# Performance work log

Hardware: AMD Instinct MI355X
Metric: run time of the kernel (lower is better)

Reference implementation:

```python
import jax, jax.numpy as jnp
import numpy as np

NUM_EMBEDDINGS = 8192
EMBEDDING_DIM = 256


def setup_inputs() -> dict:
    key = jax.random.key(0)
    k1, k2 = jax.random.split(key)
    z = jax.random.normal(k1, (16, EMBEDDING_DIM, 32, 32), dtype=jnp.float32)
    # nn.Embedding default init: N(0, 1)
    emb_table = jax.random.normal(k2, (NUM_EMBEDDINGS, EMBEDDING_DIM), dtype=jnp.float32)
    return {"z": z, "emb_table": emb_table}


def reference(z, emb_table):
    # z: [B, D, H, W]; emb_table: [K, D]
    B, D, H, W = z.shape
    # flatten to per-token vectors: [B*H*W, D]
    zf = z.reshape(B, D, H * W).transpose(0, 2, 1).reshape(B * H * W, D)
    Wt = jax.lax.stop_gradient(emb_table)  # original detaches W for distance
    # argmin of mean squared distance == argmin of squared distance;
    # expand ||z - w||^2 = ||z||^2 - 2 z.w + ||w||^2 (avoid (N,K,D) expansion)
    z_sq = jnp.sum(zf * zf, axis=-1, keepdims=True)          # [N, 1]
    w_sq = jnp.sum(Wt * Wt, axis=-1)                          # [K]
    dists = z_sq - 2.0 * (zf @ Wt.T) + w_sq                   # [N, K]
    token_ids = jnp.argmin(dists, axis=-1)                    # [N]
    quantized = emb_table[token_ids]                          # [N, D] (differentiable gather)
    return quantized.reshape(B, H * W, D).transpose(0, 2, 1).reshape(B, D, H, W)
```

## Files before the change

### kernel.cpp

```cpp
#include <hip/hip_runtime.h>
#include <stdint.h>

#define DIM 256
#define NEMB 8192
#define NTOK 16384
#define HW 1024

typedef __attribute__((ext_vector_type(4))) int int4v;

__device__ __forceinline__ void async_cp16(void* lds, const void* g) {
  __builtin_amdgcn_global_load_lds(
      (const __attribute__((address_space(1))) unsigned int*)g,
      (__attribute__((address_space(3))) unsigned int*)lds, 16, 0, 0);
}
__device__ __forceinline__ int q0_of(float x) {
  int q = __float2int_rn(x * 20.0f);
  return q > 127 ? 127 : (q < -127 ? -127 : q);
}
__device__ __forceinline__ int q1_of(float x, int q0) {
  float e = x * 20.0f - (float)q0;
  int q = __float2int_rn(e * 128.0f);
  return q > 127 ? 127 : (q < -127 ? -127 : q);
}
__device__ __forceinline__ unsigned int pack4(int a, int b, int c, int d) {
  return (unsigned int)(a & 0xff) | ((unsigned int)(b & 0xff) << 8) |
         ((unsigned int)(c & 0xff) << 16) | ((unsigned int)(d & 0xff) << 24);
}
__device__ __forceinline__ unsigned int med3u(unsigned int a, unsigned int b,
                                              unsigned int c) {
  unsigned int m;
  asm("v_med3_u32 %0, %1, %2, %3" : "=v"(m) : "v"(a), "v"(b), "v"(c));
  return m;
}
__device__ __forceinline__ void top3_insert(unsigned int v, unsigned int& m1,
                                            unsigned int& m2, unsigned int& m3) {
  unsigned int t2 = med3u(v, m1, m2);
  unsigned int t3 = med3u(v, m2, m3);
  m1 = v < m1 ? v : m1;
  m2 = t2;
  m3 = t3;
}

__global__ __launch_bounds__(256) void prep_kernel(
    const float* __restrict__ emb, unsigned int* __restrict__ q0w,
    unsigned int* __restrict__ q1w, int* __restrict__ iwsq2,
    const float* __restrict__ z, unsigned int* __restrict__ q0z) {
  __shared__ float tile[64][65];
  int tid = threadIdx.x;
  int lane = tid & 63;
  if (blockIdx.x < 2048) {
    int row = blockIdx.x * 4 + (tid >> 6);
    const float4 v = *(const float4*)(emb + (size_t)row * DIM + lane * 4);
    float s = v.x * v.x + v.y * v.y + v.z * v.z + v.w * v.w;
    int a0 = q0_of(v.x), b0 = q0_of(v.y), c0 = q0_of(v.z), d0 = q0_of(v.w);
    q0w[row * (DIM / 4) + lane] = pack4(a0, b0, c0, d0);
    q1w[row * (DIM / 4) + lane] =
        pack4(q1_of(v.x, a0), q1_of(v.y, b0), q1_of(v.z, c0), q1_of(v.w, d0));
#pragma unroll
    for (int off = 32; off > 0; off >>= 1) s += __shfl_xor(s, off, 64);
    if (lane == 0) iwsq2[row] = (int)rintf(s * 25600.0f) + 8192;
    return;
  }
  int idx = blockIdx.x - 2048;
  int b = idx >> 6, d0 = ((idx >> 4) & 3) * 64, hw0 = (idx & 15) * 64;
  int grp = tid >> 6;
  const float* src = z + (size_t)b * DIM * HW + hw0 + lane;
#pragma unroll
  for (int i = 0; i < 16; i++) {
    int dl = grp + i * 4;
    tile[dl][lane] = src[(size_t)(d0 + dl) * HW];
  }
  __syncthreads();
  int dq = tid & 15;
#pragma unroll
  for (int p = 0; p < 4; p++) {
    int n = (tid >> 4) + p * 16;
    int a0 = q0_of(tile[dq * 4 + 0][n]), b0 = q0_of(tile[dq * 4 + 1][n]);
    int c0 = q0_of(tile[dq * 4 + 2][n]), e0 = q0_of(tile[dq * 4 + 3][n]);
    int token = b * HW + hw0 + n;
    q0z[(size_t)token * (DIM / 4) + (d0 >> 2) + dq] = pack4(a0, b0, c0, e0);
  }
}

__global__ __launch_bounds__(256, 3) void gemm_topk_kernel(
    const signed char* __restrict__ q0z, const signed char* __restrict__ q0w,
    const signed char* __restrict__ q1w, const int* __restrict__ iwsq2,
    uint4* __restrict__ partials) {
  __shared__ __align__(16) signed char sB[2][4][32 * 128];

  const int bid = blockIdx.x;
  const int kq = bid & 7;
  const int tg = bid >> 3;
  const int tid = threadIdx.x;
  const int lane = tid & 63, w = tid >> 6;
  const int c = lane & 15, quad = lane >> 4;
  const int n0 = tg * 128;
  const int k0g = kq * 1024;

  int4v af0[2][4];
#pragma unroll
  for (int t = 0; t < 2; t++) {
    const size_t arow = (size_t)(n0 + w * 32 + t * 16 + c) * DIM;
#pragma unroll
    for (int s = 0; s < 4; s++)
      af0[t][s] = *(const int4v*)(q0z + arow + s * 64 + quad * 16);
  }

  const int srow = tid >> 3;
  const int scl = ((tid & 7) ^ (srow & 7)) * 16;
  const signed char* p0 = q0w + (size_t)(k0g + srow) * DIM + scl;
  const signed char* p1 = q1w + (size_t)(k0g + srow) * DIM + scl;
  async_cp16(&sB[0][0][tid * 16], p0);
  async_cp16(&sB[0][1][tid * 16], p0 + 128);
  async_cp16(&sB[0][2][tid * 16], p1);
  async_cp16(&sB[0][3][tid * 16], p1 + 128);
  p0 += 32 * DIM;
  p1 += 32 * DIM;
  __syncthreads();

  unsigned int m1[8], m2[8], m3[8];
#pragma unroll
  for (int i = 0; i < 8; i++) {
    m1[i] = 0xFFFFFFFFu; m2[i] = 0xFFFFFFFFu; m3[i] = 0xFFFFFFFFu;
  }

  unsigned int idxA = (unsigned)(k0g + c);
  const int4v zero = {0, 0, 0, 0};

  for (int it = 0; it < 32; it++) {
    const int buf = it & 1;
    if (it + 1 < 32) {
      const int nb = buf ^ 1;
      async_cp16(&sB[nb][0][tid * 16], p0);
      async_cp16(&sB[nb][1][tid * 16], p0 + 128);
      async_cp16(&sB[nb][2][tid * 16], p1);
      async_cp16(&sB[nb][3][tid * 16], p1 + 128);
      p0 += 32 * DIM;
      p1 += 32 * DIM;
    }
    const int iw0 = iwsq2[k0g + it * 32 + c];
    const int iw1 = iwsq2[k0g + it * 32 + 16 + c];

    int4v b0a[4], b0b[4];
#pragma unroll
    for (int s = 0; s < 4; s++) {
      const int ph = ((((s & 1) << 2) + quad) ^ (c & 7)) * 16;
      b0a[s] = *(const int4v*)(&sB[buf][s >> 1][c * 128 + ph]);
      b0b[s] = *(const int4v*)(&sB[buf][s >> 1][(16 + c) * 128 + ph]);
    }
    int4v a[2][2];
#pragma unroll
    for (int t = 0; t < 2; t++) {
      a[t][0] = __builtin_amdgcn_mfma_i32_16x16x64_i8(af0[t][0], b0a[0], zero, 0, 0, 0);
      a[t][1] = __builtin_amdgcn_mfma_i32_16x16x64_i8(af0[t][0], b0b[0], zero, 0, 0, 0);
#pragma unroll
      for (int s = 1; s < 4; s++) {
        a[t][0] = __builtin_amdgcn_mfma_i32_16x16x64_i8(af0[t][s], b0a[s], a[t][0], 0, 0, 0);
        a[t][1] = __builtin_amdgcn_mfma_i32_16x16x64_i8(af0[t][s], b0b[s], a[t][1], 0, 0, 0);
      }
    }
#pragma unroll
    for (int t = 0; t < 2; t++)
#pragma unroll
      for (int cn = 0; cn < 2; cn++)
#pragma unroll
        for (int r = 0; r < 4; r++) a[t][cn][r] <<= 7;
#pragma unroll
    for (int s = 0; s < 4; s++) {
      const int ph = ((((s & 1) << 2) + quad) ^ (c & 7)) * 16;
      int4v b1a = *(const int4v*)(&sB[buf][2 + (s >> 1)][c * 128 + ph]);
      int4v b1b = *(const int4v*)(&sB[buf][2 + (s >> 1)][(16 + c) * 128 + ph]);
#pragma unroll
      for (int t = 0; t < 2; t++) {
        a[t][0] = __builtin_amdgcn_mfma_i32_16x16x64_i8(af0[t][s], b1a, a[t][0], 0, 0, 0);
        a[t][1] = __builtin_amdgcn_mfma_i32_16x16x64_i8(af0[t][s], b1b, a[t][1], 0, 0, 0);
      }
    }
#pragma unroll
    for (int t = 0; t < 2; t++) {
#pragma unroll
      for (int r = 0; r < 4; r++) {
        unsigned int s0 = (unsigned int)(iw0 - a[t][0][r]);
        unsigned int s1 = (unsigned int)(iw1 - a[t][1][r]);
        s0 = s0 < 0x2000000u ? s0 : 0x1FFFFFFu;
        s1 = s1 < 0x2000000u ? s1 : 0x1FFFFFFu;
        unsigned int pk0 = ((s0 << 7) & 0xFFFFE000u) | idxA;
        unsigned int pk1 = ((s1 << 7) & 0xFFFFE000u) | (idxA + 16);
        top3_insert(pk0 < pk1 ? pk0 : pk1, m1[t * 4 + r], m2[t * 4 + r],
                    m3[t * 4 + r]);
      }
    }
    idxA += 32;
    __syncthreads();
  }

#pragma unroll
  for (int ix = 0; ix < 8; ix++) {
    unsigned int a1 = m1[ix], a2 = m2[ix], a3 = m3[ix];
#pragma unroll
    for (int off = 1; off < 16; off <<= 1) {
      unsigned int o1 = __shfl_xor(a1, off, 16);
      unsigned int o2 = __shfl_xor(a2, off, 16);
      unsigned int o3 = __shfl_xor(a3, off, 16);
      top3_insert(o1, a1, a2, a3);
      top3_insert(o2, a1, a2, a3);
      top3_insert(o3, a1, a2, a3);
    }
    m1[ix] = a1; m2[ix] = a2; m3[ix] = a3;
  }
  if (c == 0) {
#pragma unroll
    for (int t = 0; t < 2; t++) {
#pragma unroll
      for (int r = 0; r < 4; r++) {
        int token = n0 + w * 32 + t * 16 + quad * 4 + r;
        partials[(size_t)kq * NTOK + token] =
            make_uint4(m1[t * 4 + r], m2[t * 4 + r], m3[t * 4 + r], 0xFFFFFFFFu);
      }
    }
  }
}

__global__ __launch_bounds__(256) void rescore_gather_kernel(
    const uint4* __restrict__ partials, const float* __restrict__ z,
    const float* __restrict__ emb, float* __restrict__ out) {
  __shared__ float tile[32][257];
  __shared__ int sid[32];
  __shared__ int wl[32];
  __shared__ int nwl;
  const int b = blockIdx.x >> 5;
  const int hw0 = (blockIdx.x & 31) * 32;
  const int tid = threadIdx.x;
  if (tid == 0) nwl = 0;
  __syncthreads();
  {
    const int tl = tid >> 3, sub = tid & 7;
    const int token = b * HW + hw0 + tl;
    uint4 e = partials[(size_t)sub * NTOK + token];
    unsigned int m = e.x < e.y ? e.x : e.y;
    m = e.z < m ? e.z : m;
#pragma unroll
    for (int off = 1; off < 8; off <<= 1) {
      unsigned int o = __shfl_xor(m, off, 8);
      m = o < m ? o : m;
    }
    const unsigned int thr = (m >> 13) + 1536;
    int cnt = (((e.x >> 13) <= thr) ? 1 : 0) + (((e.y >> 13) <= thr) ? 1 : 0) +
              (((e.z >> 13) <= thr) ? 1 : 0);
#pragma unroll
    for (int off = 1; off < 8; off <<= 1) cnt += __shfl_xor(cnt, off, 8);
    if (sub == 0) {
      if (cnt == 1) {
        sid[tl] = (int)(m & 0x1FFFu);
      } else {
        int i = atomicAdd(&nwl, 1);
        wl[i] = tl;
      }
    }
  }
  __syncthreads();
  {
    const int w = tid >> 6, lane = tid & 63;
    for (int i = w; i < nwl; i += 4) {
      const int tl = wl[i];
      const int token = b * HW + hw0 + tl;
      unsigned int p[24];
#pragma unroll
      for (int q = 0; q < 8; q++) {
        uint4 t = partials[(size_t)q * NTOK + token];
        p[q * 3] = t.x;
        p[q * 3 + 1] = t.y;
        p[q * 3 + 2] = t.z;
      }
      unsigned int smin = p[0];
#pragma unroll
      for (int q = 1; q < 24; q++) smin = p[q] < smin ? p[q] : smin;
      const unsigned int thr = (smin >> 13) + 1536;
      float zv[4];
#pragma unroll
      for (int j = 0; j < 4; j++)
        zv[j] = z[(size_t)b * DIM * HW + (size_t)(lane * 4 + j) * HW + hw0 + tl];
      double best = 1e300;
      int bid2 = NEMB;
#pragma unroll
      for (int q = 0; q < 24; q++) {
        if ((p[q] >> 13) <= thr) {
          int id = (int)(p[q] & 0x1FFFu);
          const float4 wv = *(const float4*)(emb + (size_t)id * DIM + lane * 4);
          double s = (double)wv.x * ((double)wv.x - 2.0 * (double)zv[0]) +
                     (double)wv.y * ((double)wv.y - 2.0 * (double)zv[1]) +
                     (double)wv.z * ((double)wv.z - 2.0 * (double)zv[2]) +
                     (double)wv.w * ((double)wv.w - 2.0 * (double)zv[3]);
#pragma unroll
          for (int off = 32; off > 0; off >>= 1) s += __shfl_xor(s, off, 64);
          if (s < best || (s == best && id < bid2)) {
            best = s;
            bid2 = id;
          }
        }
      }
      if (lane == 0) sid[tl] = bid2;
    }
  }
  __syncthreads();
  for (int i = 0; i < 32; i++)
    tile[i][tid] = emb[(size_t)sid[i] * DIM + tid];
  __syncthreads();
  int h = tid & 31, dg = tid >> 5;
  for (int i = 0; i < 32; i++) {
    int d = i * 8 + dg;
    out[(size_t)b * DIM * HW + (size_t)d * HW + hw0 + h] = tile[h][d];
  }
}

extern "C" void kernel_launch(void* const* d_in, const int* in_sizes, int n_in,
                              void* d_out, int out_size, void* d_ws, size_t ws_size,
                              hipStream_t stream) {
  const float* z = (const float*)d_in[0];
  const float* emb = (const float*)d_in[1];
  float* out = (float*)d_out;
  char* ws = (char*)d_ws;

  signed char* q0w = (signed char*)(ws);
  signed char* q1w = (signed char*)(ws + 2097152);
  signed char* q0z = (signed char*)(ws + 4194304);
  int* iwsq2 = (int*)(ws + 8388608);
  uint4* partials = (uint4*)(ws + 8421376);

  prep_kernel<<<dim3(3072), 256, 0, stream>>>(
      emb, (unsigned int*)q0w, (unsigned int*)q1w, iwsq2, z, (unsigned int*)q0z);
  gemm_topk_kernel<<<dim3(1024), 256, 0, stream>>>(q0z, q0w, q1w, iwsq2,
                                                   partials);
  rescore_gather_kernel<<<dim3(512), 256, 0, stream>>>(partials, z, emb, out);
}
```

Before: 167.8 us.

## Shrink per-wave GEMM tile to 16x16 and use 512-thread blocks

Reworks the int8 MFMA distance/top-3 kernel so each wave computes a single 16-token by 16-code tile instead of 2x2 tiles. Blocks grow to 512 threads (8 waves covering 128 tokens), and the codebook step per iteration shrinks to 16 codes with one async copy per thread, so there are twice as many iterations. The aim is lower register pressure and higher occupancy (launch bounds 512,8) to hide latency. The cost is less register reuse of the A and B fragments, more LDS reads per MFMA, and twice as many barriers.

```diff
diff --git a/kernel.cpp b/kernel.cpp
--- a/kernel.cpp
+++ b/kernel.cpp
@@ -82,11 +82,11 @@
   }
 }
 
-__global__ __launch_bounds__(256, 3) void gemm_topk_kernel(
+__global__ __launch_bounds__(512, 8) void gemm_topk_kernel(
     const signed char* __restrict__ q0z, const signed char* __restrict__ q0w,
     const signed char* __restrict__ q1w, const int* __restrict__ iwsq2,
     uint4* __restrict__ partials) {
-  __shared__ __align__(16) signed char sB[2][4][32 * 128];
+  __shared__ __align__(16) signed char sB[2][4][16 * 128];
 
   const int bid = blockIdx.x;
   const int kq = bid & 7;
@@ -97,106 +97,75 @@
   const int n0 = tg * 128;
   const int k0g = kq * 1024;
 
-  int4v af0[2][4];
-#pragma unroll
-  for (int t = 0; t < 2; t++) {
-    const size_t arow = (size_t)(n0 + w * 32 + t * 16 + c) * DIM;
+  int4v af0[4];
+  {
+    const size_t arow = (size_t)(n0 + w * 16 + c) * DIM;
 #pragma unroll
     for (int s = 0; s < 4; s++)
-      af0[t][s] = *(const int4v*)(q0z + arow + s * 64 + quad * 16);
-  }
-
-  const int srow = tid >> 3;
-  const int scl = ((tid & 7) ^ (srow & 7)) * 16;
-  const signed char* p0 = q0w + (size_t)(k0g + srow) * DIM + scl;
-  const signed char* p1 = q1w + (size_t)(k0g + srow) * DIM + scl;
-  async_cp16(&sB[0][0][tid * 16], p0);
-  async_cp16(&sB[0][1][tid * 16], p0 + 128);
-  async_cp16(&sB[0][2][tid * 16], p1);
-  async_cp16(&sB[0][3][tid * 16], p1 + 128);
-  p0 += 32 * DIM;
-  p1 += 32 * DIM;
-  __syncthreads();
-
-  unsigned int m1[8], m2[8], m3[8];
-#pragma unroll
-  for (int i = 0; i < 8; i++) {
+      af0[s] = *(const int4v*)(q0z + arow + s * 64 + quad * 16);
+  }
+
+  const int arr = tid >> 7;
+  const int t2 = tid & 127;
+  const int srow = t2 >> 3;
+  const int scl = ((t2 & 7) ^ (srow & 7)) * 16;
+  const signed char* p = ((arr & 2) ? q1w : q0w) +
+                         (size_t)(k0g + srow) * DIM + (arr & 1) * 128 + scl;
+  async_cp16(&sB[0][arr][t2 * 16], p);
+  p += 16 * DIM;
+  __syncthreads();
+
+  unsigned int m1[4], m2[4], m3[4];
+#pragma unroll
+  for (int i = 0; i < 4; i++) {
     m1[i] = 0xFFFFFFFFu; m2[i] = 0xFFFFFFFFu; m3[i] = 0xFFFFFFFFu;
   }
 
   unsigned int idxA = (unsigned)(k0g + c);
   const int4v zero = {0, 0, 0, 0};
 
-  for (int it = 0; it < 32; it++) {
+  for (int it = 0; it < 64; it++) {
     const int buf = it & 1;
-    if (it + 1 < 32) {
-      const int nb = buf ^ 1;
-      async_cp16(&sB[nb][0][tid * 16], p0);
-      async_cp16(&sB[nb][1][tid * 16], p0 + 128);
-      async_cp16(&sB[nb][2][tid * 16], p1);
-      async_cp16(&sB[nb][3][tid * 16], p1 + 128);
-      p0 += 32 * DIM;
-      p1 += 32 * DIM;
-    }
-    const int iw0 = iwsq2[k0g + it * 32 + c];
-    const int iw1 = iwsq2[k0g + it * 32 + 16 + c];
-
-    int4v b0a[4], b0b[4];
+    if (it + 1 < 64) {
+      async_cp16(&sB[buf ^ 1][arr][t2 * 16], p);
+      p += 16 * DIM;
+    }
+    const int iw0 = iwsq2[k0g + it * 16 + c];
+
+    int4v acc;
+    {
+      const int ph0 = (quad ^ (c & 7)) * 16;
+      int4v b = *(const int4v*)(&sB[buf][0][c * 128 + ph0]);
+      acc = __builtin_amdgcn_mfma_i32_16x16x64_i8(af0[0], b, zero, 0, 0, 0);
+    }
+#pragma unroll
+    for (int s = 1; s < 4; s++) {
+      const int ph = ((((s & 1) << 2) + quad) ^ (c & 7)) * 16;
+      int4v b = *(const int4v*)(&sB[buf][s >> 1][c * 128 + ph]);
+      acc = __builtin_amdgcn_mfma_i32_16x16x64_i8(af0[s], b, acc, 0, 0, 0);
+    }
+#pragma unroll
+    for (int r = 0; r < 4; r++) acc[r] <<= 7;
 #pragma unroll
     for (int s = 0; s < 4; s++) {
       const int ph = ((((s & 1) << 2) + quad) ^ (c & 7)) * 16;
-      b0a[s] = *(const int4v*)(&sB[buf][s >> 1][c * 128 + ph]);
-      b0b[s] = *(const int4v*)(&sB[buf][s >> 1][(16 + c) * 128 + ph]);
-    }
-    int4v a[2][2];
-#pragma unroll
-    for (int t = 0; t < 2; t++) {
-      a[t][0] = __builtin_amdgcn_mfma_i32_16x16x64_i8(af0[t][0], b0a[0], zero, 0, 0, 0);
-      a[t][1] = __builtin_amdgcn_mfma_i32_16x16x64_i8(af0[t][0], b0b[0], zero, 0, 0, 0);
-#pragma unroll
-      for (int s = 1; s < 4; s++) {
-        a[t][0] = __builtin_amdgcn_mfma_i32_16x16x64_i8(af0[t][s], b0a[s], a[t][0], 0, 0, 0);
-        a[t][1] = __builtin_amdgcn_mfma_i32_16x16x64_i8(af0[t][s], b0b[s], a[t][1], 0, 0, 0);
-      }
-    }
-#pragma unroll
-    for (int t = 0; t < 2; t++)
-#pragma unroll
-      for (int cn = 0; cn < 2; cn++)
-#pragma unroll
-        for (int r = 0; r < 4; r++) a[t][cn][r] <<= 7;
-#pragma unroll
-    for (int s = 0; s < 4; s++) {
-      const int ph = ((((s & 1) << 2) + quad) ^ (c & 7)) * 16;
-      int4v b1a = *(const int4v*)(&sB[buf][2 + (s >> 1)][c * 128 + ph]);
-      int4v b1b = *(const int4v*)(&sB[buf][2 + (s >> 1)][(16 + c) * 128 + ph]);
-#pragma unroll
-      for (int t = 0; t < 2; t++) {
-        a[t][0] = __builtin_amdgcn_mfma_i32_16x16x64_i8(af0[t][s], b1a, a[t][0], 0, 0, 0);
-        a[t][1] = __builtin_amdgcn_mfma_i32_16x16x64_i8(af0[t][s], b1b, a[t][1], 0, 0, 0);
-      }
-    }
-#pragma unroll
-    for (int t = 0; t < 2; t++) {
-#pragma unroll
-      for (int r = 0; r < 4; r++) {
-        unsigned int s0 = (unsigned int)(iw0 - a[t][0][r]);
-        unsigned int s1 = (unsigned int)(iw1 - a[t][1][r]);
-        s0 = s0 < 0x2000000u ? s0 : 0x1FFFFFFu;
-        s1 = s1 < 0x2000000u ? s1 : 0x1FFFFFFu;
-        unsigned int pk0 = ((s0 << 7) & 0xFFFFE000u) | idxA;
-        unsigned int pk1 = ((s1 << 7) & 0xFFFFE000u) | (idxA + 16);
-        top3_insert(pk0 < pk1 ? pk0 : pk1, m1[t * 4 + r], m2[t * 4 + r],
-                    m3[t * 4 + r]);
-      }
-    }
-    idxA += 32;
+      int4v b = *(const int4v*)(&sB[buf][2 + (s >> 1)][c * 128 + ph]);
+      acc = __builtin_amdgcn_mfma_i32_16x16x64_i8(af0[s], b, acc, 0, 0, 0);
+    }
+#pragma unroll
+    for (int r = 0; r < 4; r++) {
+      unsigned int s0 = (unsigned int)(iw0 - acc[r]);
+      s0 = s0 < 0x2000000u ? s0 : 0x1FFFFFFu;
+      unsigned int pk = ((s0 << 7) & 0xFFFFE000u) | idxA;
+      top3_insert(pk, m1[r], m2[r], m3[r]);
+    }
+    idxA += 16;
     __syncthreads();
   }
 
 #pragma unroll
-  for (int ix = 0; ix < 8; ix++) {
-    unsigned int a1 = m1[ix], a2 = m2[ix], a3 = m3[ix];
+  for (int r = 0; r < 4; r++) {
+    unsigned int a1 = m1[r], a2 = m2[r], a3 = m3[r];
 #pragma unroll
     for (int off = 1; off < 16; off <<= 1) {
       unsigned int o1 = __shfl_xor(a1, off, 16);
@@ -206,17 +175,14 @@
       top3_insert(o2, a1, a2, a3);
       top3_insert(o3, a1, a2, a3);
     }
-    m1[ix] = a1; m2[ix] = a2; m3[ix] = a3;
+    m1[r] = a1; m2[r] = a2; m3[r] = a3;
   }
   if (c == 0) {
 #pragma unroll
-    for (int t = 0; t < 2; t++) {
-#pragma unroll
-      for (int r = 0; r < 4; r++) {
-        int token = n0 + w * 32 + t * 16 + quad * 4 + r;
-        partials[(size_t)kq * NTOK + token] =
-            make_uint4(m1[t * 4 + r], m2[t * 4 + r], m3[t * 4 + r], 0xFFFFFFFFu);
-      }
+    for (int r = 0; r < 4; r++) {
+      int token = n0 + w * 16 + quad * 4 + r;
+      partials[(size_t)kq * NTOK + token] =
+          make_uint4(m1[r], m2[r], m3[r], 0xFFFFFFFFu);
     }
   }
 }
@@ -329,7 +295,7 @@
 
   prep_kernel<<<dim3(3072), 256, 0, stream>>>(
       emb, (unsigned int*)q0w, (unsigned int*)q1w, iwsq2, z, (unsigned int*)q0z);
-  gemm_topk_kernel<<<dim3(1024), 256, 0, stream>>>(q0z, q0w, q1w, iwsq2,
+  gemm_topk_kernel<<<dim3(1024), 512, 0, stream>>>(q0z, q0w, q1w, iwsq2,
                                                    partials);
   rescore_gather_kernel<<<dim3(512), 256, 0, stream>>>(partials, z, emb, out);
 }
```

New measurement: 179.7 us. 7.1% more time.
